# Kernel optimization log

Hardware: AMD Instinct MI355X
Metric: run time of the kernel (lower is better)

## Reference

```python
import jax, jax.numpy as jnp
import numpy as np

D_MODEL = 1024
D_ATTN = 1024
BATCH = 4
SEQ = 2048


def setup_inputs() -> dict:
    key = jax.random.key(0)
    k_x, k_q, k_k, k_v = jax.random.split(key, 4)
    return {
        "x": jax.random.normal(k_x, (BATCH, SEQ, D_MODEL), dtype=jnp.float32),
        "Wq": jax.random.normal(k_q, (D_MODEL, D_ATTN), dtype=jnp.float32),
        "Wk": jax.random.normal(k_k, (D_MODEL, D_ATTN), dtype=jnp.float32),
        "Wv": jax.random.normal(k_v, (D_MODEL, D_ATTN), dtype=jnp.float32),
    }


def reference(x, Wq, Wk, Wv):
    # x: [B, S, D]; Wq/Wk/Wv: [D, Da]
    B, S, _ = x.shape
    Da = Wq.shape[1]
    Q = jnp.einsum("bsd,da->bsa", x, Wq)
    K = jnp.einsum("bsd,da->bsa", x, Wk)
    V = jnp.einsum("bsd,da->bsa", x, Wv)
    scores = jnp.einsum("bia,bja->bij", Q, K)  # [B, S, S]
    # Faithful to source: tril with diagonal=1 (allows attending one step ahead)
    i = jnp.arange(S)[:, None]
    j = jnp.arange(S)[None, :]
    allowed = j <= i + 1  # [S, S] bool
    scores = jnp.where(allowed[None, :, :], scores, -jnp.inf)
    scale = jnp.sqrt(jnp.asarray(Da, dtype=scores.dtype))
    attn = jax.nn.softmax(scores / scale, axis=-1)
    # dropout p=0 -> identity
    return jnp.einsum("bij,bja->bia", attn, V)
```

## Files before the change

### kernel.cpp

```cpp
#include <hip/hip_runtime.h>
#include <math.h>

#define BATCH 4
#define SEQ 2048
#define DM 1024
#define NTOK (BATCH * SEQ)
#define NE ((size_t)NTOK * DM)
#define WN ((size_t)DM * DM)

using s16x8 = __attribute__((ext_vector_type(8))) short;
using f32x4 = __attribute__((ext_vector_type(4))) float;

__device__ __forceinline__ unsigned short f2bf(float f) {
    unsigned u = __builtin_bit_cast(unsigned, f);
    u += 0x7FFFu + ((u >> 16) & 1u);
    return (unsigned short)(u >> 16);
}
__device__ __forceinline__ float bf2f(unsigned short h) {
    unsigned u = ((unsigned)h) << 16;
    return __builtin_bit_cast(float, u);
}

__device__ __forceinline__ f32x4 MFMA(s16x8 a, s16x8 b, f32x4 c) {
    return __builtin_amdgcn_mfma_f32_16x16x32_bf16(a, b, c, 0, 0, 0);
}

#define AS1 __attribute__((address_space(1)))
#define AS3 __attribute__((address_space(3)))
__device__ __forceinline__ void gll16(const void* g, void* l) {
    __builtin_amdgcn_global_load_lds((const AS1 void*)g, (AS3 void*)l, 16, 0, 0);
}

__device__ __forceinline__ s16x8 lds_frag(const short* base, int row, int g) {
    return *(const s16x8*)(base + row * 64 + ((g ^ (row & 7)) << 3));
}

__device__ __forceinline__ void stage_tile(const unsigned short* g0, size_t rs,
                                           short* lds, int tid) {
    int lane = tid & 63, w = tid >> 6;
    #pragma unroll
    for (int c = 0; c < 4; ++c) {
        int s = c * 256 + w * 64 + lane;
        int row = s >> 3, gg = s & 7;
        int graw = gg ^ (row & 7);
        gll16(g0 + (size_t)row * rs + graw * 8, lds + (size_t)s * 8);
    }
}

__global__ __launch_bounds__(256) void split_x(const float* __restrict__ x,
                                               unsigned short* __restrict__ xh,
                                               unsigned short* __restrict__ xl) {
    size_t n4 = NE / 4;
    for (size_t i = (size_t)blockIdx.x * 256 + threadIdx.x; i < n4;
         i += (size_t)gridDim.x * 256) {
        float4 v = ((const float4*)x)[i];
        ushort4 h, l;
        h.x = f2bf(v.x); l.x = f2bf(v.x - bf2f(h.x));
        h.y = f2bf(v.y); l.y = f2bf(v.y - bf2f(h.y));
        h.z = f2bf(v.z); l.z = f2bf(v.z - bf2f(h.z));
        h.w = f2bf(v.w); l.w = f2bf(v.w - bf2f(h.w));
        ((ushort4*)xh)[i] = h;
        ((ushort4*)xl)[i] = l;
    }
}

__global__ __launch_bounds__(256) void split_wt(const float* __restrict__ Wq,
                                                const float* __restrict__ Wk,
                                                const float* __restrict__ Wv,
                                                unsigned short* __restrict__ Wsp) {
    const int z = blockIdx.z;
    const float* W = (z == 0) ? Wq : (z == 1) ? Wk : Wv;
    unsigned short* oh = Wsp + (size_t)z * 2 * WN;
    unsigned short* ol = oh + WN;

    __shared__ float t[64][65];
    const int d0 = blockIdx.x * 64, n0 = blockIdx.y * 64;
    const int tid = threadIdx.x;
    #pragma unroll
    for (int c = 0; c < 16; ++c) {
        int f = c * 256 + tid; int r = f >> 6, cc = f & 63;
        t[r][cc] = W[(size_t)(d0 + r) * DM + n0 + cc];
    }
    __syncthreads();
    #pragma unroll
    for (int c = 0; c < 16; ++c) {
        int f = c * 256 + tid; int r = f >> 6, cc = f & 63;
        float v = t[cc][r];
        unsigned short h = f2bf(v);
        size_t o = (size_t)(n0 + r) * DM + d0 + cc;
        oh[o] = h;
        ol[o] = f2bf(v - bf2f(h));
    }
}

__global__ __launch_bounds__(256, 2) void qk_mfma(
    const unsigned short* __restrict__ xh, const unsigned short* __restrict__ xl,
    const unsigned short* __restrict__ Wsp,
    unsigned short* __restrict__ Qh, unsigned short* __restrict__ Ql,
    unsigned short* __restrict__ Kh, unsigned short* __restrict__ Kl) {
    const int z = blockIdx.z;
    const unsigned short* Wh = Wsp + (size_t)z * 2 * WN;
    const unsigned short* Wl = Wh + WN;
    unsigned short* Ch = z ? Kh : Qh;
    unsigned short* Cl = z ? Kl : Ql;

    const int m0 = blockIdx.x * 128, n0 = blockIdx.y * 128;
    __shared__ short Ah[128 * 64], Al[128 * 64], Bh[128 * 64], Bl[128 * 64];
    const int tid = threadIdx.x, lane = tid & 63, w = tid >> 6;
    const int wr = w >> 1, wc = w & 1;

    f32x4 acc[4][4];
    #pragma unroll
    for (int i = 0; i < 4; ++i)
        #pragma unroll
        for (int j = 0; j < 4; ++j) acc[i][j] = (f32x4){0.f, 0.f, 0.f, 0.f};

    for (int k0 = 0; k0 < DM; k0 += 64) {
        stage_tile(xh + (size_t)m0 * DM + k0, DM, Ah, tid);
        stage_tile(xl + (size_t)m0 * DM + k0, DM, Al, tid);
        stage_tile(Wh + (size_t)n0 * DM + k0, DM, Bh, tid);
        stage_tile(Wl + (size_t)n0 * DM + k0, DM, Bl, tid);
        __syncthreads();
        #pragma unroll
        for (int ks = 0; ks < 2; ++ks) {
            const int g = ks * 4 + (lane >> 4);
            s16x8 a_h[4], a_l[4], b_h[4], b_l[4];
            #pragma unroll
            for (int mi = 0; mi < 4; ++mi) {
                int r = wr * 64 + mi * 16 + (lane & 15);
                a_h[mi] = lds_frag(Ah, r, g);
                a_l[mi] = lds_frag(Al, r, g);
            }
            #pragma unroll
            for (int ni = 0; ni < 4; ++ni) {
                int r = wc * 64 + ni * 16 + (lane & 15);
                b_h[ni] = lds_frag(Bh, r, g);
                b_l[ni] = lds_frag(Bl, r, g);
            }
            #pragma unroll
            for (int mi = 0; mi < 4; ++mi)
                #pragma unroll
                for (int ni = 0; ni < 4; ++ni) {
                    acc[mi][ni] = MFMA(a_h[mi], b_h[ni], acc[mi][ni]);
                    acc[mi][ni] = MFMA(a_h[mi], b_l[ni], acc[mi][ni]);
                    acc[mi][ni] = MFMA(a_l[mi], b_h[ni], acc[mi][ni]);
                }
        }
        __syncthreads();
    }
    #pragma unroll
    for (int mi = 0; mi < 4; ++mi)
        #pragma unroll
        for (int ni = 0; ni < 4; ++ni)
            #pragma unroll
            for (int r = 0; r < 4; ++r) {
                int row = m0 + wr * 64 + mi * 16 + (lane >> 4) * 4 + r;
                int col = n0 + wc * 64 + ni * 16 + (lane & 15);
                float v = acc[mi][ni][r];
                unsigned short h = f2bf(v);
                size_t o = (size_t)row * DM + col;
                Ch[o] = h;
                Cl[o] = f2bf(v - bf2f(h));
            }
}

__global__ __launch_bounds__(256, 2) void vt_mfma(
    const unsigned short* __restrict__ Wsp, const unsigned short* __restrict__ xh,
    unsigned short* __restrict__ Vt) {
    const unsigned short* Wvh = Wsp + 4 * WN;
    const int m0 = blockIdx.x * 128;
    const int n0 = blockIdx.y * 128;
    __shared__ short Ah[128 * 64], Bh[128 * 64];
    const int tid = threadIdx.x, lane = tid & 63, w = tid >> 6;
    const int wr = w >> 1, wc = w & 1;

    f32x4 acc[4][4];
    #pragma unroll
    for (int i = 0; i < 4; ++i)
        #pragma unroll
        for (int j = 0; j < 4; ++j) acc[i][j] = (f32x4){0.f, 0.f, 0.f, 0.f};

    for (int k0 = 0; k0 < DM; k0 += 64) {
        stage_tile(Wvh + (size_t)m0 * DM + k0, DM, Ah, tid);
        stage_tile(xh + (size_t)n0 * DM + k0, DM, Bh, tid);
        __syncthreads();
        #pragma unroll
        for (int ks = 0; ks < 2; ++ks) {
            const int g = ks * 4 + (lane >> 4);
            s16x8 a_h[4], b_h[4];
            #pragma unroll
            for (int mi = 0; mi < 4; ++mi)
                a_h[mi] = lds_frag(Ah, wr * 64 + mi * 16 + (lane & 15), g);
            #pragma unroll
            for (int ni = 0; ni < 4; ++ni)
                b_h[ni] = lds_frag(Bh, wc * 64 + ni * 16 + (lane & 15), g);
            #pragma unroll
            for (int mi = 0; mi < 4; ++mi)
                #pragma unroll
                for (int ni = 0; ni < 4; ++ni)
                    acc[mi][ni] = MFMA(a_h[mi], b_h[ni], acc[mi][ni]);
        }
        __syncthreads();
    }
    #pragma unroll
    for (int mi = 0; mi < 4; ++mi)
        #pragma unroll
        for (int ni = 0; ni < 4; ++ni)
            #pragma unroll
            for (int r = 0; r < 4; ++r) {
                int row = m0 + wr * 64 + mi * 16 + (lane >> 4) * 4 + r;
                int col = n0 + wc * 64 + ni * 16 + (lane & 15);
                Vt[(size_t)row * NTOK + col] = f2bf(acc[mi][ni][r]);
            }
}

__global__ __launch_bounds__(256, 2) void scores_mfma(
    const unsigned short* __restrict__ Qh, const unsigned short* __restrict__ Ql,
    const unsigned short* __restrict__ Kh, const unsigned short* __restrict__ Kl,
    float* __restrict__ P) {
    const int jt = blockIdx.x, t = blockIdx.y, b = blockIdx.z;
    if (jt > t + 1) return;
    const int m0 = t * 128, n0 = jt * 128;
    const size_t qrow0 = (size_t)b * SEQ + m0;
    const size_t krow0 = (size_t)b * SEQ + n0;

    __shared__ short Ah[128 * 64], Al[128 * 64], Bh[128 * 64], Bl[128 * 64];
    const int tid = threadIdx.x, lane = tid & 63, w = tid >> 6;
    const int wr = w >> 1, wc = w & 1;

    f32x4 acc[4][4];
    #pragma unroll
    for (int i = 0; i < 4; ++i)
        #pragma unroll
        for (int j = 0; j < 4; ++j) acc[i][j] = (f32x4){0.f, 0.f, 0.f, 0.f};

    for (int k0 = 0; k0 < DM; k0 += 64) {
        stage_tile(Qh + qrow0 * DM + k0, DM, Ah, tid);
        stage_tile(Ql + qrow0 * DM + k0, DM, Al, tid);
        stage_tile(Kh + krow0 * DM + k0, DM, Bh, tid);
        stage_tile(Kl + krow0 * DM + k0, DM, Bl, tid);
        __syncthreads();
        #pragma unroll
        for (int ks = 0; ks < 2; ++ks) {
            const int g = ks * 4 + (lane >> 4);
            s16x8 a_h[4], a_l[4], b_h[4], b_l[4];
            #pragma unroll
            for (int mi = 0; mi < 4; ++mi) {
                int r = wr * 64 + mi * 16 + (lane & 15);
                a_h[mi] = lds_frag(Ah, r, g);
                a_l[mi] = lds_frag(Al, r, g);
            }
            #pragma unroll
            for (int ni = 0; ni < 4; ++ni) {
                int r = wc * 64 + ni * 16 + (lane & 15);
                b_h[ni] = lds_frag(Bh, r, g);
                b_l[ni] = lds_frag(Bl, r, g);
            }
            #pragma unroll
            for (int mi = 0; mi < 4; ++mi)
                #pragma unroll
                for (int ni = 0; ni < 4; ++ni) {
                    acc[mi][ni] = MFMA(a_h[mi], b_h[ni], acc[mi][ni]);
                    acc[mi][ni] = MFMA(a_h[mi], b_l[ni], acc[mi][ni]);
                    acc[mi][ni] = MFMA(a_l[mi], b_h[ni], acc[mi][ni]);
                }
        }
        __syncthreads();
    }
    const float scale = 1.0f / 32.0f;
    #pragma unroll
    for (int mi = 0; mi < 4; ++mi)
        #pragma unroll
        for (int ni = 0; ni < 4; ++ni)
            #pragma unroll
            for (int r = 0; r < 4; ++r) {
                int i = m0 + wr * 64 + mi * 16 + (lane >> 4) * 4 + r;
                int j = n0 + wc * 64 + ni * 16 + (lane & 15);
                float v = (j <= i + 1) ? acc[mi][ni][r] * scale : -INFINITY;
                P[((size_t)b * SEQ + i) * SEQ + j] = v;
            }
}

__global__ __launch_bounds__(256) void softmax_bf16(
    const float* __restrict__ P, unsigned short* __restrict__ P2) {
    const int row = blockIdx.x;
    const int b = row >> 11, i = row & (SEQ - 1);
    const int t = i >> 7;
    const int L = min(SEQ, (t + 2) * 128);
    const float* p = P + ((size_t)b * SEQ + i) * SEQ;
    unsigned short* q = P2 + ((size_t)b * SEQ + i) * SEQ;
    const int tid = threadIdx.x;
    __shared__ float red[4];

    float v[8];
    #pragma unroll
    for (int c = 0; c < 8; ++c) {
        int j = c * 256 + tid;
        v[c] = (j < L) ? p[j] : -INFINITY;
    }
    float m = -INFINITY;
    #pragma unroll
    for (int c = 0; c < 8; ++c) m = fmaxf(m, v[c]);
    #pragma unroll
    for (int o = 32; o > 0; o >>= 1) m = fmaxf(m, __shfl_xor(m, o));
    if ((tid & 63) == 0) red[tid >> 6] = m;
    __syncthreads();
    m = fmaxf(fmaxf(red[0], red[1]), fmaxf(red[2], red[3]));
    __syncthreads();

    float s = 0.f;
    #pragma unroll
    for (int c = 0; c < 8; ++c) { v[c] = __expf(v[c] - m); s += v[c]; }
    #pragma unroll
    for (int o = 32; o > 0; o >>= 1) s += __shfl_xor(s, o);
    if ((tid & 63) == 0) red[tid >> 6] = s;
    __syncthreads();
    s = red[0] + red[1] + red[2] + red[3];
    const float inv = 1.f / s;

    #pragma unroll
    for (int c = 0; c < 8; ++c) {
        int j = c * 256 + tid;
        if (j < L) q[j] = f2bf(v[c] * inv);
    }
}

__global__ __launch_bounds__(256, 2) void pv_mfma(
    const unsigned short* __restrict__ P2, const unsigned short* __restrict__ Vt,
    float* __restrict__ Out) {
    const int bx = blockIdx.x, t = blockIdx.y, b = blockIdx.z;
    const int m0 = t * 128, n0 = bx * 128;
    const int jlim = min(SEQ, (t + 2) * 128);

    __shared__ short Pa[128 * 64], Vb[128 * 64];
    const int tid = threadIdx.x, lane = tid & 63, w = tid >> 6;
    const int wr = w >> 1, wc = w & 1;

    f32x4 acc[4][4];
    #pragma unroll
    for (int i = 0; i < 4; ++i)
        #pragma unroll
        for (int j = 0; j < 4; ++j) acc[i][j] = (f32x4){0.f, 0.f, 0.f, 0.f};

    for (int k0 = 0; k0 < jlim; k0 += 64) {
        stage_tile(P2 + ((size_t)b * SEQ + m0) * SEQ + k0, SEQ, Pa, tid);
        stage_tile(Vt + (size_t)n0 * NTOK + (size_t)b * SEQ + k0, NTOK, Vb, tid);
        __syncthreads();
        #pragma unroll
        for (int ks = 0; ks < 2; ++ks) {
            const int g = ks * 4 + (lane >> 4);
            s16x8 a_h[4], b_h[4];
            #pragma unroll
            for (int mi = 0; mi < 4; ++mi)
                a_h[mi] = lds_frag(Pa, wr * 64 + mi * 16 + (lane & 15), g);
            #pragma unroll
            for (int ni = 0; ni < 4; ++ni)
                b_h[ni] = lds_frag(Vb, wc * 64 + ni * 16 + (lane & 15), g);
            #pragma unroll
            for (int mi = 0; mi < 4; ++mi)
                #pragma unroll
                for (int ni = 0; ni < 4; ++ni)
                    acc[mi][ni] = MFMA(a_h[mi], b_h[ni], acc[mi][ni]);
        }
        __syncthreads();
    }
    #pragma unroll
    for (int mi = 0; mi < 4; ++mi)
        #pragma unroll
        for (int ni = 0; ni < 4; ++ni)
            #pragma unroll
            for (int r = 0; r < 4; ++r) {
                int i = m0 + wr * 64 + mi * 16 + (lane >> 4) * 4 + r;
                int col = n0 + wc * 64 + ni * 16 + (lane & 15);
                Out[((size_t)b * SEQ + i) * DM + col] = acc[mi][ni][r];
            }
}

extern "C" void kernel_launch(void* const* d_in, const int* in_sizes, int n_in,
                              void* d_out, int out_size, void* d_ws, size_t ws_size,
                              hipStream_t stream) {
    const float* x  = (const float*)d_in[0];
    const float* Wq = (const float*)d_in[1];
    const float* Wk = (const float*)d_in[2];
    const float* Wv = (const float*)d_in[3];

    char* ws = (char*)d_ws;
    unsigned short* Kh = (unsigned short*)ws;
    unsigned short* Kl = Kh + NE;
    unsigned short* Vt = Kl + NE;
    float* P = (float*)(ws + 6 * NE);
    unsigned short* P2 = (unsigned short*)ws;
    unsigned short* xh  = (unsigned short*)(ws + 6 * NE);
    unsigned short* xl  = xh + NE;
    unsigned short* Wsp = (unsigned short*)(ws + 10 * NE);
    unsigned short* Qh = (unsigned short*)d_out;
    unsigned short* Ql = Qh + NE;

    split_x<<<2048, 256, 0, stream>>>(x, xh, xl);
    {
        dim3 g(16, 16, 3);
        split_wt<<<g, 256, 0, stream>>>(Wq, Wk, Wv, Wsp);
    }
    {
        dim3 g(NTOK / 128, DM / 128, 2);
        qk_mfma<<<g, 256, 0, stream>>>(xh, xl, Wsp, Qh, Ql, Kh, Kl);
    }
    {
        dim3 g(DM / 128, NTOK / 128, 1);
        vt_mfma<<<g, 256, 0, stream>>>(Wsp, xh, Vt);
    }
    {
        dim3 g(16, 16, 4);
        scores_mfma<<<g, 256, 0, stream>>>(Qh, Ql, Kh, Kl, P);
    }
    softmax_bf16<<<BATCH * SEQ, 256, 0, stream>>>(P, P2);
    {
        dim3 g(DM / 128, 16, 4);
        pv_mfma<<<g, 256, 0, stream>>>(P2, Vt, (float*)d_out);
    }
}
```

Measured before the change: 324.0 us.

## Precompute Wq·Wkᵀ and compute scores as (x·M)·xᵀ instead of Q·Kᵀ

Reassociates the score computation: it forms M = Wq·Wkᵀ once (a 1024x1024 GEMM), then Y = x·M, and computes scores as Y·xᵀ. This drops the separate K projection GEMM over all tokens, replacing it with a small weight-weight GEMM, and avoids transposing Wq/Wk by splitting them directly. It relies on D_attn equal to D_model, so the same work count is kept for Y, and it changes the rounding path of the split-bf16 arithmetic.

```diff
diff --git a/kernel.cpp b/kernel.cpp
--- a/kernel.cpp
+++ b/kernel.cpp
@@ -64,46 +64,52 @@
     }
 }
 
-__global__ __launch_bounds__(256) void split_wt(const float* __restrict__ Wq,
-                                                const float* __restrict__ Wk,
-                                                const float* __restrict__ Wv,
-                                                unsigned short* __restrict__ Wsp) {
+__global__ __launch_bounds__(256) void split_w(
+    const float* __restrict__ Wq, const float* __restrict__ Wk,
+    const float* __restrict__ Wv,
+    unsigned short* __restrict__ Wqh, unsigned short* __restrict__ Wql,
+    unsigned short* __restrict__ Wkh, unsigned short* __restrict__ Wkl,
+    unsigned short* __restrict__ Wvt) {
     const int z = blockIdx.z;
-    const float* W = (z == 0) ? Wq : (z == 1) ? Wk : Wv;
-    unsigned short* oh = Wsp + (size_t)z * 2 * WN;
-    unsigned short* ol = oh + WN;
-
-    __shared__ float t[64][65];
-    const int d0 = blockIdx.x * 64, n0 = blockIdx.y * 64;
     const int tid = threadIdx.x;
-    #pragma unroll
-    for (int c = 0; c < 16; ++c) {
-        int f = c * 256 + tid; int r = f >> 6, cc = f & 63;
-        t[r][cc] = W[(size_t)(d0 + r) * DM + n0 + cc];
-    }
-    __syncthreads();
-    #pragma unroll
-    for (int c = 0; c < 16; ++c) {
-        int f = c * 256 + tid; int r = f >> 6, cc = f & 63;
-        float v = t[cc][r];
-        unsigned short h = f2bf(v);
-        size_t o = (size_t)(n0 + r) * DM + d0 + cc;
-        oh[o] = h;
-        ol[o] = f2bf(v - bf2f(h));
-    }
-}
-
-__global__ __launch_bounds__(256, 2) void qk_mfma(
-    const unsigned short* __restrict__ xh, const unsigned short* __restrict__ xl,
-    const unsigned short* __restrict__ Wsp,
-    unsigned short* __restrict__ Qh, unsigned short* __restrict__ Ql,
-    unsigned short* __restrict__ Kh, unsigned short* __restrict__ Kl) {
-    const int z = blockIdx.z;
-    const unsigned short* Wh = Wsp + (size_t)z * 2 * WN;
-    const unsigned short* Wl = Wh + WN;
-    unsigned short* Ch = z ? Kh : Qh;
-    unsigned short* Cl = z ? Kl : Ql;
-
+    if (z < 2) {
+        const float* W = z ? Wk : Wq;
+        unsigned short* oh = z ? Wkh : Wqh;
+        unsigned short* ol = z ? Wkl : Wql;
+        size_t n4 = WN / 4;
+        size_t stride = (size_t)gridDim.x * gridDim.y * 256;
+        for (size_t i = ((size_t)blockIdx.y * gridDim.x + blockIdx.x) * 256 + tid;
+             i < n4; i += stride) {
+            float4 v = ((const float4*)W)[i];
+            ushort4 h, l;
+            h.x = f2bf(v.x); l.x = f2bf(v.x - bf2f(h.x));
+            h.y = f2bf(v.y); l.y = f2bf(v.y - bf2f(h.y));
+            h.z = f2bf(v.z); l.z = f2bf(v.z - bf2f(h.z));
+            h.w = f2bf(v.w); l.w = f2bf(v.w - bf2f(h.w));
+            ((ushort4*)oh)[i] = h;
+            ((ushort4*)ol)[i] = l;
+        }
+    } else {
+        __shared__ float t[64][65];
+        const int d0 = blockIdx.x * 64, n0 = blockIdx.y * 64;
+        #pragma unroll
+        for (int c = 0; c < 16; ++c) {
+            int f = c * 256 + tid; int r = f >> 6, cc = f & 63;
+            t[r][cc] = Wv[(size_t)(d0 + r) * DM + n0 + cc];
+        }
+        __syncthreads();
+        #pragma unroll
+        for (int c = 0; c < 16; ++c) {
+            int f = c * 256 + tid; int r = f >> 6, cc = f & 63;
+            Wvt[(size_t)(n0 + r) * DM + d0 + cc] = f2bf(t[cc][r]);
+        }
+    }
+}
+
+__global__ __launch_bounds__(256, 2) void gemm3_split(
+    const unsigned short* __restrict__ Ah_, const unsigned short* __restrict__ Al_,
+    const unsigned short* __restrict__ Bh_, const unsigned short* __restrict__ Bl_,
+    unsigned short* __restrict__ Ch, unsigned short* __restrict__ Cl) {
     const int m0 = blockIdx.x * 128, n0 = blockIdx.y * 128;
     __shared__ short Ah[128 * 64], Al[128 * 64], Bh[128 * 64], Bl[128 * 64];
     const int tid = threadIdx.x, lane = tid & 63, w = tid >> 6;
@@ -116,10 +122,10 @@
         for (int j = 0; j < 4; ++j) acc[i][j] = (f32x4){0.f, 0.f, 0.f, 0.f};
 
     for (int k0 = 0; k0 < DM; k0 += 64) {
-        stage_tile(xh + (size_t)m0 * DM + k0, DM, Ah, tid);
-        stage_tile(xl + (size_t)m0 * DM + k0, DM, Al, tid);
-        stage_tile(Wh + (size_t)n0 * DM + k0, DM, Bh, tid);
-        stage_tile(Wl + (size_t)n0 * DM + k0, DM, Bl, tid);
+        stage_tile(Ah_ + (size_t)m0 * DM + k0, DM, Ah, tid);
+        stage_tile(Al_ + (size_t)m0 * DM + k0, DM, Al, tid);
+        stage_tile(Bh_ + (size_t)n0 * DM + k0, DM, Bh, tid);
+        stage_tile(Bl_ + (size_t)n0 * DM + k0, DM, Bl, tid);
         __syncthreads();
         #pragma unroll
         for (int ks = 0; ks < 2; ++ks) {
@@ -165,9 +171,8 @@
 }
 
 __global__ __launch_bounds__(256, 2) void vt_mfma(
-    const unsigned short* __restrict__ Wsp, const unsigned short* __restrict__ xh,
+    const unsigned short* __restrict__ Wvt, const unsigned short* __restrict__ xh,
     unsigned short* __restrict__ Vt) {
-    const unsigned short* Wvh = Wsp + 4 * WN;
     const int m0 = blockIdx.x * 128;
     const int n0 = blockIdx.y * 128;
     __shared__ short Ah[128 * 64], Bh[128 * 64];
@@ -181,7 +186,7 @@
         for (int j = 0; j < 4; ++j) acc[i][j] = (f32x4){0.f, 0.f, 0.f, 0.f};
 
     for (int k0 = 0; k0 < DM; k0 += 64) {
-        stage_tile(Wvh + (size_t)m0 * DM + k0, DM, Ah, tid);
+        stage_tile(Wvt + (size_t)m0 * DM + k0, DM, Ah, tid);
         stage_tile(xh + (size_t)n0 * DM + k0, DM, Bh, tid);
         __syncthreads();
         #pragma unroll
@@ -215,8 +220,8 @@
 }
 
 __global__ __launch_bounds__(256, 2) void scores_mfma(
-    const unsigned short* __restrict__ Qh, const unsigned short* __restrict__ Ql,
-    const unsigned short* __restrict__ Kh, const unsigned short* __restrict__ Kl,
+    const unsigned short* __restrict__ Yh, const unsigned short* __restrict__ Yl,
+    const unsigned short* __restrict__ xh, const unsigned short* __restrict__ xl,
     float* __restrict__ P) {
     const int jt = blockIdx.x, t = blockIdx.y, b = blockIdx.z;
     if (jt > t + 1) return;
@@ -235,10 +240,10 @@
         for (int j = 0; j < 4; ++j) acc[i][j] = (f32x4){0.f, 0.f, 0.f, 0.f};
 
     for (int k0 = 0; k0 < DM; k0 += 64) {
-        stage_tile(Qh + qrow0 * DM + k0, DM, Ah, tid);
-        stage_tile(Ql + qrow0 * DM + k0, DM, Al, tid);
-        stage_tile(Kh + krow0 * DM + k0, DM, Bh, tid);
-        stage_tile(Kl + krow0 * DM + k0, DM, Bl, tid);
+        stage_tile(Yh + qrow0 * DM + k0, DM, Ah, tid);
+        stage_tile(Yl + qrow0 * DM + k0, DM, Al, tid);
+        stage_tile(xh + krow0 * DM + k0, DM, Bh, tid);
+        stage_tile(xl + krow0 * DM + k0, DM, Bl, tid);
         __syncthreads();
         #pragma unroll
         for (int ks = 0; ks < 2; ++ks) {
@@ -385,33 +390,41 @@
     const float* Wv = (const float*)d_in[3];
 
     char* ws = (char*)d_ws;
-    unsigned short* Kh = (unsigned short*)ws;
-    unsigned short* Kl = Kh + NE;
-    unsigned short* Vt = Kl + NE;
+    unsigned short* Vt = (unsigned short*)ws;
+    unsigned short* xh = (unsigned short*)(ws + 2 * NE);
+    unsigned short* xl = (unsigned short*)(ws + 4 * NE);
     float* P = (float*)(ws + 6 * NE);
-    unsigned short* P2 = (unsigned short*)ws;
-    unsigned short* xh  = (unsigned short*)(ws + 6 * NE);
-    unsigned short* xl  = xh + NE;
-    unsigned short* Wsp = (unsigned short*)(ws + 10 * NE);
-    unsigned short* Qh = (unsigned short*)d_out;
-    unsigned short* Ql = Qh + NE;
+    unsigned short* P2 = (unsigned short*)(ws + 2 * NE);
+    unsigned short* Wqh = (unsigned short*)(ws + 6 * NE);
+    unsigned short* Wql = Wqh + WN;
+    unsigned short* Wkh = Wql + WN;
+    unsigned short* Wkl = Wkh + WN;
+    unsigned short* Mh  = Wkl + WN;
+    unsigned short* Ml  = Mh + WN;
+    unsigned short* Wvt = Ml + WN;
+    unsigned short* Yh = (unsigned short*)d_out;
+    unsigned short* Yl = Yh + NE;
 
     split_x<<<2048, 256, 0, stream>>>(x, xh, xl);
     {
         dim3 g(16, 16, 3);
-        split_wt<<<g, 256, 0, stream>>>(Wq, Wk, Wv, Wsp);
-    }
-    {
-        dim3 g(NTOK / 128, DM / 128, 2);
-        qk_mfma<<<g, 256, 0, stream>>>(xh, xl, Wsp, Qh, Ql, Kh, Kl);
-    }
-    {
-        dim3 g(DM / 128, NTOK / 128, 1);
-        vt_mfma<<<g, 256, 0, stream>>>(Wsp, xh, Vt);
+        split_w<<<g, 256, 0, stream>>>(Wq, Wk, Wv, Wqh, Wql, Wkh, Wkl, Wvt);
+    }
+    {
+        dim3 g(8, 8);
+        gemm3_split<<<g, 256, 0, stream>>>(Wkh, Wkl, Wqh, Wql, Mh, Ml);
+    }
+    {
+        dim3 g(NTOK / 128, DM / 128);
+        gemm3_split<<<g, 256, 0, stream>>>(xh, xl, Mh, Ml, Yh, Yl);
+    }
+    {
+        dim3 g(DM / 128, NTOK / 128);
+        vt_mfma<<<g, 256, 0, stream>>>(Wvt, xh, Vt);
     }
     {
         dim3 g(16, 16, 4);
-        scores_mfma<<<g, 256, 0, stream>>>(Qh, Ql, Kh, Kl, P);
+        scores_mfma<<<g, 256, 0, stream>>>(Yh, Yl, xh, xl, P);
     }
     softmax_bf16<<<BATCH * SEQ, 256, 0, stream>>>(P, P2);
     {
```

Result: no change. 324.4 us (+0.1%).
